# Optimization experiments

Hardware: AMD Instinct MI355X
Metric: run time of the kernel (lower is better)

Reference implementation:

```python
import jax, jax.numpy as jnp
import numpy as np

BATCH_SIZE = 4096
N_VIEWS = 2
NUM_GPU = 1
TEMPERATURE = 0.07
FEAT_DIM = 128
N = (BATCH_SIZE // NUM_GPU) * N_VIEWS  # 8192


def setup_inputs() -> dict:
    key = jax.random.key(0)
    features = jax.random.normal(key, (N, FEAT_DIM), dtype=jnp.float32)
    return {"features": features}


def reference(features):
    n = features.shape[0]
    b = BATCH_SIZE // NUM_GPU
    # labels: [arange(b)] * n_views concatenated -> pairwise equality matrix
    lbl_vec = jnp.tile(jnp.arange(b), N_VIEWS)            # [N]
    lab = lbl_vec[None, :] == lbl_vec[:, None]            # [N, N] bool

    # F.normalize(dim=1): divide by L2 norm clamped at 1e-12
    norm = jnp.linalg.norm(features, axis=1, keepdims=True)
    f = features / jnp.maximum(norm, 1e-12)
    sim = f @ f.T                                          # [N, N]

    # Remove diagonal: row i keeps columns j != i in original order.
    cols = jnp.arange(n - 1)
    off_idx = cols[None, :] + (cols[None, :] >= jnp.arange(n)[:, None])  # [N, N-1]
    sim_od = jnp.take_along_axis(sim, off_idx, axis=1)     # [N, N-1]
    lab_od = jnp.take_along_axis(lab, off_idx, axis=1)     # [N, N-1] bool

    # Stable sort: positives (label True) first, preserving original column order,
    # matching torch's masked-select + concat([positives, negatives]).
    order = jnp.argsort(~lab_od, axis=1, stable=True)      # [N, N-1]
    logits = jnp.take_along_axis(sim_od, order, axis=1) / TEMPERATURE

    # CrossEntropyLoss with target class 0 (mean reduction)
    loss = -jax.nn.log_softmax(logits, axis=1)[:, 0]
    return loss.mean()
```

## Files before the change

### kernel.cpp

```cpp
#include <hip/hip_runtime.h>
#include <hip/hip_bf16.h>
#include <cstdint>

#define NROWS 8192
#define FDIM  128
#define HALF_N 4096

typedef short bf16x8 __attribute__((ext_vector_type(8)));
typedef float f32x4  __attribute__((ext_vector_type(4)));

#define K1 (1.4426950408889634f / 0.07f)

#if __has_builtin(__builtin_amdgcn_exp2f)
#define EXP2(x) __builtin_amdgcn_exp2f(x)
#else
#define EXP2(x) exp2f(x)
#endif


__global__ void __launch_bounds__(256) normalize_kernel(const float* __restrict__ f,
                                                        short* __restrict__ packed,
                                                        float* __restrict__ esum_g) {
    const int row  = blockIdx.x * 4 + (threadIdx.x >> 6);
    const int lane = threadIdx.x & 63;
    const float2 v = ((const float2*)(f + (size_t)row * FDIM))[lane];
    float ss = v.x * v.x + v.y * v.y;
    #pragma unroll
    for (int m = 1; m < 64; m <<= 1) ss += __shfl_xor(ss, m);
    const float scale = 1.0f / fmaxf(sqrtf(ss), 1e-12f);

    const int off = ((((row >> 4) * 4 + (lane >> 4)) * 64)
                     + ((lane >> 2) & 3) * 16 + (row & 15)) * 8 + 2 * (lane & 3);
    __hip_bfloat16 b0 = __float2bfloat16(v.x * scale);
    __hip_bfloat16 b1 = __float2bfloat16(v.y * scale);
    unsigned u = (unsigned)*(unsigned short*)&b0
               | ((unsigned)*(unsigned short*)&b1 << 16);
    *(unsigned*)(packed + off) = u;

    if (threadIdx.x < 4) esum_g[blockIdx.x * 4 + threadIdx.x] = 0.0f;
}

__device__ __forceinline__ float2 bf2_to_f2(unsigned u) {
    return make_float2(__uint_as_float(u << 16),
                       __uint_as_float(u & 0xffff0000u));
}

__global__ void __launch_bounds__(256, 4) sim_kernel(const short* __restrict__ pk,
                                                     float* __restrict__ esum_g,
                                                     float* __restrict__ pos_g,
                                                     float* __restrict__ diag_g) {
    if (blockIdx.x >= 1024) {
        const int i  = (blockIdx.x - 1024) * 256 + threadIdx.x;
        const int ip = i ^ HALF_N;
        const uint4* P = (const uint4*)pk;
        float dot = 0.f, self = 0.f;
        #pragma unroll
        for (int cc = 0; cc < 16; cc++) {
            const uint4 a = P[((i  >> 4) * 4 + (cc >> 2)) * 64 + (cc & 3) * 16 + (i  & 15)];
            const uint4 b = P[((ip >> 4) * 4 + (cc >> 2)) * 64 + (cc & 3) * 16 + (ip & 15)];
            const unsigned au[4] = {a.x, a.y, a.z, a.w};
            const unsigned bu[4] = {b.x, b.y, b.z, b.w};
            #pragma unroll
            for (int q = 0; q < 4; q++) {
                const float2 av = bf2_to_f2(au[q]);
                const float2 bv = bf2_to_f2(bu[q]);
                dot  = __builtin_fmaf(av.x, bv.x, __builtin_fmaf(av.y, bv.y, dot));
                self = __builtin_fmaf(av.x, av.x, __builtin_fmaf(av.y, av.y, self));
            }
        }
        pos_g[i]  = dot;
        diag_g[i] = EXP2(__builtin_fmaf(self, K1, -K1));
        return;
    }

    const int tid   = threadIdx.x;
    const int w     = tid >> 6;
    const int lane  = tid & 63;
    const int quad  = lane >> 4;
    const int l16   = lane & 15;
    const int j     = blockIdx.x & 15;
    const int strip = (blockIdx.x >> 4) * 4 + w;
    const bf16x8* P = (const bf16x8*)pk;

    bf16x8 a_reg[4][2];
    #pragma unroll
    for (int fr = 0; fr < 2; fr++)
        #pragma unroll
        for (int ks = 0; ks < 4; ks++)
            a_reg[ks][fr] = P[(((strip * 2 + fr) * 4) + ks) * 64 + lane];

    float ep[2][4];
    #pragma unroll
    for (int a = 0; a < 2; a++)
        #pragma unroll
        for (int b = 0; b < 4; b++) ep[a][b] = 0.0f;

    const int cb0 = j * 32;

    #pragma unroll 8
    for (int cb = 0; cb < 32; cb++) {
        bf16x8 b[4];
        #pragma unroll
        for (int ks = 0; ks < 4; ks++)
            b[ks] = P[((cb0 + cb) * 4 + ks) * 64 + lane];

        f32x4 acc[2];
        #pragma unroll
        for (int fr = 0; fr < 2; fr++) acc[fr] = (f32x4){0.f, 0.f, 0.f, 0.f};
        #pragma unroll
        for (int ks = 0; ks < 4; ks++)
            #pragma unroll
            for (int fr = 0; fr < 2; fr++)
                acc[fr] = __builtin_amdgcn_mfma_f32_16x16x32_bf16(
                              a_reg[ks][fr], b[ks], acc[fr], 0, 0, 0);

        #pragma unroll
        for (int fr = 0; fr < 2; fr++)
            #pragma unroll
            for (int r = 0; r < 4; r++)
                ep[fr][r] += EXP2(__builtin_fmaf(acc[fr][r], K1, -K1));
    }

    #pragma unroll
    for (int fr = 0; fr < 2; fr++)
        #pragma unroll
        for (int r = 0; r < 4; r++) {
            float v = ep[fr][r];
            #pragma unroll
            for (int m = 1; m < 16; m <<= 1) v += __shfl_xor(v, m);
            if (l16 == 0)
                atomicAdd(&esum_g[strip * 32 + fr * 16 + quad * 4 + r], v);
        }
}

__global__ void __launch_bounds__(256) final_kernel(const float* __restrict__ esum_g,
                                                    const float* __restrict__ pos_g,
                                                    const float* __restrict__ diag_g,
                                                    float* __restrict__ out) {
    const int tid = threadIdx.x;
    const float invT = 1.0f / 0.07f;
    float acc = 0.0f;
    for (int i = tid; i < NROWS; i += 256)
        acc += logf(esum_g[i] - diag_g[i]) + invT - pos_g[i] * invT;
    #pragma unroll
    for (int m = 1; m < 64; m <<= 1) acc += __shfl_xor(acc, m);
    __shared__ float ws[4];
    if ((tid & 63) == 0) ws[tid >> 6] = acc;
    __syncthreads();
    if (tid == 0) out[0] = (ws[0] + ws[1] + ws[2] + ws[3]) * (1.0f / (float)NROWS);
}

extern "C" void kernel_launch(void* const* d_in, const int* in_sizes, int n_in,
                              void* d_out, int out_size, void* d_ws, size_t ws_size,
                              hipStream_t stream) {
    const float* features = (const float*)d_in[0];
    float* out = (float*)d_out;

    char* ws = (char*)d_ws;
    short* packed = (short*)ws;
    float* esum_g = (float*)(ws + 2097152);
    float* pos_g  = (float*)(ws + 2097152 + 32768);
    float* diag_g = (float*)(ws + 2097152 + 65536);

    normalize_kernel<<<NROWS / 4, 256, 0, stream>>>(features, packed, esum_g);

    sim_kernel<<<1024 + NROWS / 256, 256, 0, stream>>>(packed, esum_g, pos_g, diag_g);

    final_kernel<<<1, 256, 0, stream>>>(esum_g, pos_g, diag_g, out);
}
```

Measured before the change: 89.34 us.

## Switch sim kernel to 32x32x16 bf16 MFMA with matching packed layout

```diff
diff --git a/kernel.cpp b/kernel.cpp
--- a/kernel.cpp
+++ b/kernel.cpp
@@ -7,7 +7,7 @@
 #define HALF_N 4096
 
 typedef short bf16x8 __attribute__((ext_vector_type(8)));
-typedef float f32x4  __attribute__((ext_vector_type(4)));
+typedef float f32x16 __attribute__((ext_vector_type(16)));
 
 #define K1 (1.4426950408889634f / 0.07f)
 
@@ -29,8 +29,8 @@
     for (int m = 1; m < 64; m <<= 1) ss += __shfl_xor(ss, m);
     const float scale = 1.0f / fmaxf(sqrtf(ss), 1e-12f);
 
-    const int off = ((((row >> 4) * 4 + (lane >> 4)) * 64)
-                     + ((lane >> 2) & 3) * 16 + (row & 15)) * 8 + 2 * (lane & 3);
+    const int off = ((((row >> 5) * 8 + (lane >> 3)) * 64)
+                     + ((lane >> 2) & 1) * 32 + (row & 31)) * 8 + 2 * (lane & 3);
     __hip_bfloat16 b0 = __float2bfloat16(v.x * scale);
     __hip_bfloat16 b1 = __float2bfloat16(v.y * scale);
     unsigned u = (unsigned)*(unsigned short*)&b0
@@ -56,8 +56,8 @@
         float dot = 0.f, self = 0.f;
         #pragma unroll
         for (int cc = 0; cc < 16; cc++) {
-            const uint4 a = P[((i  >> 4) * 4 + (cc >> 2)) * 64 + (cc & 3) * 16 + (i  & 15)];
-            const uint4 b = P[((ip >> 4) * 4 + (cc >> 2)) * 64 + (cc & 3) * 16 + (ip & 15)];
+            const uint4 a = P[((i  >> 5) * 8 + (cc >> 1)) * 64 + (cc & 1) * 32 + (i  & 31)];
+            const uint4 b = P[((ip >> 5) * 8 + (cc >> 1)) * 64 + (cc & 1) * 32 + (ip & 31)];
             const unsigned au[4] = {a.x, a.y, a.z, a.w};
             const unsigned bu[4] = {b.x, b.y, b.z, b.w};
             #pragma unroll
@@ -76,61 +76,50 @@
     const int tid   = threadIdx.x;
     const int w     = tid >> 6;
     const int lane  = tid & 63;
-    const int quad  = lane >> 4;
-    const int l16   = lane & 15;
+    const int half  = lane >> 5;
+    const int l32   = lane & 31;
     const int j     = blockIdx.x & 15;
     const int strip = (blockIdx.x >> 4) * 4 + w;
     const bf16x8* P = (const bf16x8*)pk;
 
-    bf16x8 a_reg[4][2];
+    bf16x8 a_reg[8];
     #pragma unroll
-    for (int fr = 0; fr < 2; fr++)
+    for (int ks = 0; ks < 8; ks++)
+        a_reg[ks] = P[(strip * 8 + ks) * 64 + lane];
+
+    float ep[16];
+    #pragma unroll
+    for (int r = 0; r < 16; r++) ep[r] = 0.0f;
+
+    const int cb0 = j * 16;
+
+    #pragma unroll 4
+    for (int cb = 0; cb < 16; cb++) {
+        bf16x8 b[8];
         #pragma unroll
-        for (int ks = 0; ks < 4; ks++)
-            a_reg[ks][fr] = P[(((strip * 2 + fr) * 4) + ks) * 64 + lane];
+        for (int ks = 0; ks < 8; ks++)
+            b[ks] = P[((cb0 + cb) * 8 + ks) * 64 + lane];
 
-    float ep[2][4];
-    #pragma unroll
-    for (int a = 0; a < 2; a++)
+        f32x16 acc = {0.f, 0.f, 0.f, 0.f, 0.f, 0.f, 0.f, 0.f,
+                      0.f, 0.f, 0.f, 0.f, 0.f, 0.f, 0.f, 0.f};
         #pragma unroll
-        for (int b = 0; b < 4; b++) ep[a][b] = 0.0f;
-
-    const int cb0 = j * 32;
-
-    #pragma unroll 8
-    for (int cb = 0; cb < 32; cb++) {
-        bf16x8 b[4];
-        #pragma unroll
-        for (int ks = 0; ks < 4; ks++)
-            b[ks] = P[((cb0 + cb) * 4 + ks) * 64 + lane];
-
-        f32x4 acc[2];
-        #pragma unroll
-        for (int fr = 0; fr < 2; fr++) acc[fr] = (f32x4){0.f, 0.f, 0.f, 0.f};
-        #pragma unroll
-        for (int ks = 0; ks < 4; ks++)
-            #pragma unroll
-            for (int fr = 0; fr < 2; fr++)
-                acc[fr] = __builtin_amdgcn_mfma_f32_16x16x32_bf16(
-                              a_reg[ks][fr], b[ks], acc[fr], 0, 0, 0);
+        for (int ks = 0; ks < 8; ks++)
+            acc = __builtin_amdgcn_mfma_f32_32x32x16_bf16(a_reg[ks], b[ks],
+                                                          acc, 0, 0, 0);
 
         #pragma unroll
-        for (int fr = 0; fr < 2; fr++)
-            #pragma unroll
-            for (int r = 0; r < 4; r++)
-                ep[fr][r] += EXP2(__builtin_fmaf(acc[fr][r], K1, -K1));
+        for (int r = 0; r < 16; r++)
+            ep[r] += EXP2(__builtin_fmaf(acc[r], K1, -K1));
     }
 
     #pragma unroll
-    for (int fr = 0; fr < 2; fr++)
+    for (int r = 0; r < 16; r++) {
+        float v = ep[r];
         #pragma unroll
-        for (int r = 0; r < 4; r++) {
-            float v = ep[fr][r];
-            #pragma unroll
-            for (int m = 1; m < 16; m <<= 1) v += __shfl_xor(v, m);
-            if (l16 == 0)
-                atomicAdd(&esum_g[strip * 32 + fr * 16 + quad * 4 + r], v);
-        }
+        for (int m = 1; m < 32; m <<= 1) v += __shfl_xor(v, m);
+        if (l32 == 0)
+            atomicAdd(&esum_g[strip * 32 + (r & 3) + 8 * (r >> 2) + 4 * half], v);
+    }
 }
 
 __global__ void __launch_bounds__(256) final_kernel(const float* __restrict__ esum_g,
```

Result: slower. 93.27 us (+4.4%).
